# Kernel optimization log

Measured on AMD Instinct MI355X. Metric: run time of the kernel, lower is better.

Reference implementation:

```python
import jax, jax.numpy as jnp
import numpy as np

NUM_HEADS = 4
NUM_GROUPS = 8
EPS = 1e-5


def group_norm(x, w, b):
    # x: [B, C, H, W], 8 groups, per-channel affine
    B, C, H, W = x.shape
    g = x.reshape(B, NUM_GROUPS, C // NUM_GROUPS, H, W)
    mu = g.mean(axis=(2, 3, 4), keepdims=True)
    var = g.var(axis=(2, 3, 4), keepdims=True)
    g = (g - mu) * jax.lax.rsqrt(var + EPS)
    x = g.reshape(B, C, H, W)
    return x * w[None, :, None, None] + b[None, :, None, None]


def setup_inputs() -> dict:
    key = jax.random.key(0)
    ks = jax.random.split(key, 7)
    B, C, H, W = 16, 256, 32, 32
    x = jax.random.normal(ks[0], (B, C, H, W), dtype=jnp.float32)
    norm_w = jnp.ones((C,), jnp.float32)
    norm_b = jnp.zeros((C,), jnp.float32)
    # 1x1 convs == channel matmuls; fan-in scaled init
    qkv_w = jax.random.normal(ks[1], (3 * C, C), dtype=jnp.float32) / np.sqrt(C)
    qkv_b = jnp.zeros((3 * C,), jnp.float32)
    proj_w = jax.random.normal(ks[2], (C, C), dtype=jnp.float32) / np.sqrt(C)
    proj_b = jnp.zeros((C,), jnp.float32)
    return {"x": x, "norm_w": norm_w, "norm_b": norm_b,
            "qkv_w": qkv_w, "qkv_b": qkv_b,
            "proj_w": proj_w, "proj_b": proj_b}


def reference(x, norm_w, norm_b, qkv_w, qkv_b, proj_w, proj_b):
    B, C, H, W = x.shape
    nh = NUM_HEADS
    d = C // nh
    N = H * W

    h = group_norm(x, norm_w, norm_b)
    # 1x1 conv -> channel matmul: [B, 3C, H, W]
    qkv = jnp.einsum('oc,bchw->bohw', qkv_w, h) + qkv_b[None, :, None, None]
    qkv = qkv.reshape(B, 3, nh, d, N)
    q, k, v = qkv[:, 0], qkv[:, 1], qkv[:, 2]  # [B, nh, d, N]

    scale = d ** (-0.5)
    attn = jnp.einsum('bhcn,bhcm->bhnm', q, k) * scale  # [B, nh, N, N]
    attn = jax.nn.softmax(attn, axis=-1)
    out = jnp.einsum('bhnm,bhcm->bhcn', attn, v)  # [B, nh, d, N]
    out = out.reshape(B, C, H, W)
    out = jnp.einsum('oc,bchw->bohw', proj_w, out) + proj_b[None, :, None, None]
    return x + out
```

## Files before the change

kernel.cpp:

```cpp
#include <hip/hip_runtime.h>
#include <math.h>

#define BATCH 16
#define CH 256
#define NG 8
#define NH 4
#define HD 64
#define NN 1024
#define GSZ 32
#define GELEMS (GSZ * NN)

typedef __attribute__((ext_vector_type(8))) __bf16 bf16x8;
typedef __attribute__((ext_vector_type(4))) __bf16 bf16x4;
typedef __attribute__((ext_vector_type(4))) _Float16 f16x4;
typedef __attribute__((ext_vector_type(4))) float f32x4;

__device__ __forceinline__ unsigned short f2b(float f) {
    union { __bf16 h; unsigned short u; } c; c.h = (__bf16)f; return c.u;
}
__device__ __forceinline__ unsigned short f2h(float f) {
    union { _Float16 h; unsigned short u; } c; c.h = (_Float16)f; return c.u;
}

#define MFMA(a, b, c) __builtin_amdgcn_mfma_f32_16x16x32_bf16(a, b, c, 0, 0, 0)
#define MFMA16(a, b, c) __builtin_amdgcn_mfma_f32_16x16x16f16(a, b, c, 0, 0, 0)

__global__ __launch_bounds__(256) void gnw_kernel(
    const float* __restrict__ x, const float* __restrict__ w,
    const float* __restrict__ bb, const float* __restrict__ qkv_w,
    const float* __restrict__ proj_w, unsigned short* __restrict__ hT,
    unsigned short* __restrict__ wq, unsigned short* __restrict__ wp)
{
    int tid = threadIdx.x;
    if (blockIdx.x >= 128) {
        int t = (blockIdx.x - 128) * 256 + tid;
        const float* src; unsigned short* dst; size_t off;
        if (t < 24576) { src = qkv_w; dst = wq; off = (size_t)t * 8; }
        else           { src = proj_w; dst = wp; off = (size_t)(t - 24576) * 8; }
        const float4* s4 = (const float4*)(src + off);
        float4 a = s4[0], b = s4[1];
        bf16x8 pk;
        pk[0] = (__bf16)a.x; pk[1] = (__bf16)a.y; pk[2] = (__bf16)a.z; pk[3] = (__bf16)a.w;
        pk[4] = (__bf16)b.x; pk[5] = (__bf16)b.y; pk[6] = (__bf16)b.z; pk[7] = (__bf16)b.w;
        *(bf16x8*)(dst + off) = pk;
        return;
    }
    const int b = blockIdx.x >> 3, g = blockIdx.x & 7;
    const float* xb = x + ((size_t)b * CH + g * GSZ) * NN;
    const float4* x4 = (const float4*)xb;

    float s = 0.f, ss = 0.f;
    #pragma unroll
    for (int i = 0; i < 32; ++i) {
        float4 v = x4[tid + i * 256];
        s  += v.x + v.y + v.z + v.w;
        ss += v.x * v.x + v.y * v.y + v.z * v.z + v.w * v.w;
    }
    #pragma unroll
    for (int off = 1; off < 64; off <<= 1) {
        s  += __shfl_xor(s, off);
        ss += __shfl_xor(ss, off);
    }
    __shared__ float red[8];
    int wave = tid >> 6, lane = tid & 63;
    if (lane == 0) { red[wave] = s; red[4 + wave] = ss; }
    __syncthreads();
    if (tid == 0) {
        float ts  = red[0] + red[1] + red[2] + red[3];
        float tss = red[4] + red[5] + red[6] + red[7];
        float mu  = ts * (1.f / GELEMS);
        float var = tss * (1.f / GELEMS) - mu * mu;
        red[0] = mu; red[1] = rsqrtf(var + 1e-5f);
    }
    __syncthreads();
    const float mu = red[0], rs = red[1];

    const int co = tid & 3;
    float wcv[8], bcv[8];
    #pragma unroll
    for (int j = 0; j < 8; ++j) {
        int c = g * GSZ + co * 8 + j;
        wcv[j] = w[c] * rs;
        bcv[j] = bb[c] - mu * wcv[j];
    }
    __shared__ float Ts[32][66];
    const int cs = tid >> 3, q = tid & 7;
    const int n_l = tid >> 2;
    for (int nt = 0; nt < 16; ++nt) {
        const float2* src = (const float2*)(xb + (size_t)cs * NN + nt * 64 + q * 8);
        #pragma unroll
        for (int t = 0; t < 4; ++t)
            *(float2*)&Ts[cs][q * 8 + t * 2] = src[t];
        __syncthreads();
        bf16x8 pk;
        #pragma unroll
        for (int j = 0; j < 8; ++j)
            pk[j] = (__bf16)(Ts[co * 8 + j][n_l] * wcv[j] + bcv[j]);
        *(bf16x8*)(hT + ((size_t)b * NN + nt * 64 + n_l) * CH + g * GSZ + co * 8) = pk;
        __syncthreads();
    }
}

template <int KIND>
__global__ __launch_bounds__(256) void gemm_kernel(
    const unsigned short* __restrict__ AT,
    const unsigned short* __restrict__ Wb,
    const float* __restrict__ bias,
    unsigned short* __restrict__ outT, unsigned short* __restrict__ outV,
    const float* __restrict__ res, float* __restrict__ out)
{
    __shared__ __align__(16) unsigned short Ws[64][136];
    __shared__ __align__(16) unsigned short Hs[64][136];
    const int b = blockIdx.z, o0 = blockIdx.y * 64, n0 = blockIdx.x * 64;
    const int tid = threadIdx.x;
    const int lane = tid & 63, wv = tid >> 6;
    const int l = lane & 15, quad = lane >> 4;
    const int iw = wv & 1, jw = wv >> 1;
    const bool qk_mode = (KIND == 0) && (blockIdx.y < 8);
    const bool v_mode  = (KIND == 0) && (blockIdx.y >= 8);
    const int r4 = tid >> 2, c4 = tid & 3;

    f32x4 acc[2][2] = {};
    for (int st = 0; st < 2; ++st) {
        const int cc0 = st * 128;
        #pragma unroll
        for (int i = 0; i < 4; ++i) {
            int ch = c4 + i * 4;
            *(bf16x8*)&Ws[r4][ch * 8] =
                *(const bf16x8*)(Wb + (size_t)(o0 + r4) * CH + cc0 + ch * 8);
            *(bf16x8*)&Hs[r4][ch * 8] =
                *(const bf16x8*)(AT + ((size_t)b * NN + n0 + r4) * CH + cc0 + ch * 8);
        }
        __syncthreads();
        #pragma unroll
        for (int kt = 0; kt < 4; ++kt) {
            bf16x8 af[2], bf[2];
            #pragma unroll
            for (int i = 0; i < 2; ++i)
                af[i] = *(const bf16x8*)&Hs[iw * 32 + i * 16 + l][kt * 32 + quad * 8];
            #pragma unroll
            for (int j = 0; j < 2; ++j)
                bf[j] = *(const bf16x8*)&Ws[jw * 32 + j * 16 + l][kt * 32 + quad * 8];
            #pragma unroll
            for (int i = 0; i < 2; ++i)
                #pragma unroll
                for (int j = 0; j < 2; ++j)
                    acc[i][j] = v_mode ? MFMA(af[i], bf[j], acc[i][j])
                                       : MFMA(bf[j], af[i], acc[i][j]);
        }
        __syncthreads();
    }

    unsigned short* Cs = (unsigned short*)Ws;
    if (qk_mode) {
        #pragma unroll
        for (int i = 0; i < 2; ++i)
            #pragma unroll
            for (int j = 0; j < 2; ++j) {
                int o_p = jw * 32 + j * 16 + quad * 4;
                int n_l = iw * 32 + i * 16 + l;
                bf16x4 pk;
                #pragma unroll
                for (int r = 0; r < 4; ++r)
                    pk[r] = (__bf16)(acc[i][j][r] + bias[o0 + o_p + r]);
                *(bf16x4*)&Cs[n_l * 72 + o_p] = pk;
            }
        __syncthreads();
        int rr = tid >> 2, ch = tid & 3;
        bf16x8 a0 = *(const bf16x8*)&Cs[rr * 72 + ch * 16];
        bf16x8 a1 = *(const bf16x8*)&Cs[rr * 72 + ch * 16 + 8];
        unsigned short* dst = outT + ((size_t)b * NN + n0 + rr) * 512 + o0 + ch * 16;
        *(bf16x8*)dst = a0;
        *(bf16x8*)(dst + 8) = a1;
    } else if (v_mode) {
        #pragma unroll
        for (int i = 0; i < 2; ++i)
            #pragma unroll
            for (int j = 0; j < 2; ++j) {
                int n_p = iw * 32 + i * 16 + quad * 4;
                int o_l = jw * 32 + j * 16 + l;
                float bs = bias[o0 + o_l];
                f16x4 pk;
                #pragma unroll
                for (int r = 0; r < 4; ++r)
                    pk[r] = (_Float16)(acc[i][j][r] + bs);
                *(f16x4*)&Cs[o_l * 72 + n_p] = pk;
            }
        __syncthreads();
        int rr = tid >> 2, ch = tid & 3;
        bf16x8 a0 = *(const bf16x8*)&Cs[rr * 72 + ch * 16];
        bf16x8 a1 = *(const bf16x8*)&Cs[rr * 72 + ch * 16 + 8];
        unsigned short* dst = outV + ((size_t)b * CH + (o0 + rr - 512)) * NN + n0 + ch * 16;
        *(bf16x8*)dst = a0;
        *(bf16x8*)(dst + 8) = a1;
    } else {
        #pragma unroll
        for (int i = 0; i < 2; ++i)
            #pragma unroll
            for (int j = 0; j < 2; ++j) {
                int o = o0 + jw * 32 + j * 16 + quad * 4;
                int n = n0 + iw * 32 + i * 16 + l;
                #pragma unroll
                for (int r = 0; r < 4; ++r) {
                    size_t idx = ((size_t)b * CH + o + r) * NN + n;
                    out[idx] = acc[i][j][r] + bias[o + r] + res[idx];
                }
            }
    }
}

__global__ __launch_bounds__(256, 4) void attn_kernel(
    const unsigned short* __restrict__ qkvT,
    const unsigned short* __restrict__ vbuf,
    unsigned short* __restrict__ ctxT)
{
    __shared__ __align__(16) unsigned short KV[2][8192];
    __shared__ float Lred[2][32];
    const int id = blockIdx.x;
    const int bh = id & 63, nt = id >> 6;
    const int b = bh >> 2, hh = bh & 3;
    const int n0 = nt * 64;
    const int tid = threadIdx.x;
    const int lane = tid & 63, w = tid >> 6;
    const int l = lane & 15, quad = lane >> 4;
    const int qx = w & 1, ky = w >> 1;
    const float KL2E = 0.125f * 1.44269504f;
    const int r4 = tid >> 2, c4 = tid & 3;

    bf16x8 qf[2][2];
    {
        const unsigned short* qp = qkvT + ((size_t)b * NN + n0 + 32 * qx + l) * 512 + hh * 64;
        #pragma unroll
        for (int ns = 0; ns < 2; ++ns)
            #pragma unroll
            for (int kt = 0; kt < 2; ++kt)
                qf[ns][kt] = *(const bf16x8*)(qp + (size_t)ns * 16 * 512 + kt * 32 + quad * 8);
    }

    const unsigned short* gk = qkvT + ((size_t)b * NN + r4) * 512 + 256 + hh * 64;
    const unsigned short* gv = vbuf + ((size_t)b * CH + hh * 64 + r4) * NN;
    const int p0 = (c4 ^ (r4 & 7)) * 8, p1 = ((c4 + 4) ^ (r4 & 7)) * 8;

    bf16x8 kpre0, kpre1, vpre0, vpre1;
    kpre0 = *(const bf16x8*)(gk + c4 * 8);
    kpre1 = *(const bf16x8*)(gk + (c4 + 4) * 8);
    vpre0 = *(const bf16x8*)(gv + c4 * 8);
    vpre1 = *(const bf16x8*)(gv + (c4 + 4) * 8);
    *(bf16x8*)&KV[0][r4 * 64 + p0] = kpre0;
    *(bf16x8*)&KV[0][r4 * 64 + p1] = kpre1;
    *(bf16x8*)&KV[0][4096 + r4 * 64 + p0] = vpre0;
    *(bf16x8*)&KV[0][4096 + r4 * 64 + p1] = vpre1;
    __syncthreads();

    float l_w[2] = {0.f, 0.f};
    f32x4 oacc[2][4] = {};

    for (int mt = 0; mt < 16; ++mt) {
        const int cur = mt & 1;
        if (mt < 15) {
            const unsigned short* gk1 = gk + (size_t)(mt + 1) * 64 * 512;
            const unsigned short* gv1 = gv + (mt + 1) * 64;
            kpre0 = *(const bf16x8*)(gk1 + c4 * 8);
            kpre1 = *(const bf16x8*)(gk1 + (c4 + 4) * 8);
            vpre0 = *(const bf16x8*)(gv1 + c4 * 8);
            vpre1 = *(const bf16x8*)(gv1 + (c4 + 4) * 8);
        }

        bf16x8 kf[2][2];
        #pragma unroll
        for (int mt2 = 0; mt2 < 2; ++mt2)
            #pragma unroll
            for (int kt = 0; kt < 2; ++kt)
                kf[mt2][kt] = *(const bf16x8*)
                    &KV[cur][(32 * ky + 16 * mt2 + l) * 64 + (((kt * 4 + quad) ^ (l & 7)) * 8)];

        f32x4 sacc[2][2] = {};
        #pragma unroll
        for (int kt = 0; kt < 2; ++kt)
            #pragma unroll
            for (int mt2 = 0; mt2 < 2; ++mt2)
                #pragma unroll
                for (int ns = 0; ns < 2; ++ns)
                    sacc[mt2][ns] = MFMA(kf[mt2][kt], qf[ns][kt], sacc[mt2][ns]);

        f16x4 pf[2][2];
        #pragma unroll
        for (int mt2 = 0; mt2 < 2; ++mt2)
            #pragma unroll
            for (int ns = 0; ns < 2; ++ns)
                #pragma unroll
                for (int r = 0; r < 4; ++r) {
                    float p = exp2f(sacc[mt2][ns][r] * KL2E);
                    l_w[ns] += p;
                    pf[mt2][ns][r] = (_Float16)p;
                }

        #pragma unroll
        for (int mt2 = 0; mt2 < 2; ++mt2) {
            const int q8 = 4 * ky + 2 * mt2 + (quad >> 1);
            const int vo = ((q8 ^ (l & 7)) * 8) + (quad & 1) * 4;
            #pragma unroll
            for (int ct = 0; ct < 4; ++ct) {
                f16x4 va = *(const f16x4*)&KV[cur][4096 + (16 * ct + l) * 64 + vo];
                #pragma unroll
                for (int ns = 0; ns < 2; ++ns)
                    oacc[ns][ct] = MFMA16(va, pf[mt2][ns], oacc[ns][ct]);
            }
        }

        if (mt < 15) {
            const int nxt = cur ^ 1;
            *(bf16x8*)&KV[nxt][r4 * 64 + p0] = kpre0;
            *(bf16x8*)&KV[nxt][r4 * 64 + p1] = kpre1;
            *(bf16x8*)&KV[nxt][4096 + r4 * 64 + p0] = vpre0;
            *(bf16x8*)&KV[nxt][4096 + r4 * 64 + p1] = vpre1;
            __syncthreads();
        }
    }

    #pragma unroll
    for (int ns = 0; ns < 2; ++ns) {
        l_w[ns] += __shfl_xor(l_w[ns], 16);
        l_w[ns] += __shfl_xor(l_w[ns], 32);
    }
    float* Ored = (float*)&KV[0][0];
    if (ky == 1) {
        #pragma unroll
        for (int ns = 0; ns < 2; ++ns) {
            if (quad == 0) Lred[qx][ns * 16 + l] = l_w[ns];
            #pragma unroll
            for (int ct = 0; ct < 4; ++ct)
                #pragma unroll
                for (int r = 0; r < 4; ++r)
                    Ored[qx * 2048 + (16 * ct + quad * 4 + r) * 32 + ns * 16 + l] =
                        oacc[ns][ct][r];
        }
    }
    __syncthreads();
    if (ky == 0) {
        unsigned short* cb = ctxT + ((size_t)b * NN + n0 + 32 * qx) * CH + hh * 64;
        #pragma unroll
        for (int ns = 0; ns < 2; ++ns) {
            float inv = 1.f / (l_w[ns] + Lred[qx][ns * 16 + l]);
            #pragma unroll
            for (int ct = 0; ct < 4; ++ct) {
                bf16x4 pk;
                #pragma unroll
                for (int r = 0; r < 4; ++r)
                    pk[r] = (__bf16)((oacc[ns][ct][r] +
                             Ored[qx * 2048 + (16 * ct + quad * 4 + r) * 32 + ns * 16 + l]) * inv);
                *(bf16x4*)(cb + (size_t)(ns * 16 + l) * CH + 16 * ct + quad * 4) = pk;
            }
        }
    }
}

extern "C" void kernel_launch(void* const* d_in, const int* in_sizes, int n_in,
                              void* d_out, int out_size, void* d_ws, size_t ws_size,
                              hipStream_t stream)
{
    const float* x      = (const float*)d_in[0];
    const float* norm_w = (const float*)d_in[1];
    const float* norm_b = (const float*)d_in[2];
    const float* qkv_w  = (const float*)d_in[3];
    const float* qkv_b  = (const float*)d_in[4];
    const float* proj_w = (const float*)d_in[5];
    const float* proj_b = (const float*)d_in[6];
    float* out = (float*)d_out;

    unsigned short* hT   = (unsigned short*)d_ws;
    unsigned short* qkvT = hT   + (size_t)BATCH * NN * CH;
    unsigned short* vbuf = qkvT + (size_t)BATCH * NN * 512;
    unsigned short* ctxT = vbuf + (size_t)BATCH * CH * NN;
    unsigned short* wq   = ctxT + (size_t)BATCH * NN * CH;
    unsigned short* wp   = wq + (size_t)768 * CH;

    gnw_kernel<<<dim3(256), 256, 0, stream>>>(x, norm_w, norm_b, qkv_w, proj_w, hT, wq, wp);
    gemm_kernel<0><<<dim3(NN / 64, 12, BATCH), 256, 0, stream>>>(
        hT, wq, qkv_b, qkvT, vbuf, nullptr, nullptr);
    attn_kernel<<<dim3(1024), 256, 0, stream>>>(qkvT, vbuf, ctxT);
    gemm_kernel<1><<<dim3(NN / 64, 4, BATCH), 256, 0, stream>>>(
        ctxT, wp, proj_b, nullptr, nullptr, x, out);
}
```

Before: 145.8 us.

## Split QKV GEMM into dedicated kernel with 128-row tiles and XOR-swizzled LDS

Replaces the templated GEMM with a dedicated QKV kernel that uses 128x64 output tiles over four 64-wide K chunks, staging operands in XOR-swizzled shared memory instead of padded rows. This halves the grid along N, doubles weight reuse per block and is meant to cut LDS bank conflicts. The group-norm transpose now stages with float4 loads into a 68-wide pad. The cost is more accumulators per thread and fewer blocks in flight.

```diff
diff --git a/kernel.cpp b/kernel.cpp
--- a/kernel.cpp
+++ b/kernel.cpp
@@ -83,14 +83,13 @@
         wcv[j] = w[c] * rs;
         bcv[j] = bb[c] - mu * wcv[j];
     }
-    __shared__ float Ts[32][66];
+    __shared__ float Ts[32][68];
     const int cs = tid >> 3, q = tid & 7;
     const int n_l = tid >> 2;
     for (int nt = 0; nt < 16; ++nt) {
-        const float2* src = (const float2*)(xb + (size_t)cs * NN + nt * 64 + q * 8);
-        #pragma unroll
-        for (int t = 0; t < 4; ++t)
-            *(float2*)&Ts[cs][q * 8 + t * 2] = src[t];
+        const float4* src = (const float4*)(xb + (size_t)cs * NN + nt * 64 + q * 8);
+        *(float4*)&Ts[cs][q * 8]     = src[0];
+        *(float4*)&Ts[cs][q * 8 + 4] = src[1];
         __syncthreads();
         bf16x8 pk;
         #pragma unroll
@@ -101,12 +100,111 @@
     }
 }
 
-template <int KIND>
-__global__ __launch_bounds__(256) void gemm_kernel(
+__global__ __launch_bounds__(256) void gemm_qkv(
     const unsigned short* __restrict__ AT,
     const unsigned short* __restrict__ Wb,
     const float* __restrict__ bias,
-    unsigned short* __restrict__ outT, unsigned short* __restrict__ outV,
+    unsigned short* __restrict__ outT, unsigned short* __restrict__ outV)
+{
+    __shared__ __align__(16) unsigned short S[128 * 64 + 64 * 64];
+    unsigned short* As = S;
+    unsigned short* Wl = S + 128 * 64;
+    const int b = blockIdx.z, o0 = blockIdx.y * 64, n0 = blockIdx.x * 128;
+    const int tid = threadIdx.x;
+    const int lane = tid & 63, w = tid >> 6;
+    const int l = lane & 15, quad = lane >> 4;
+    const int iw = w & 1, jw = w >> 1;
+    const bool qk_mode = (blockIdx.y < 8);
+    const int sr = tid >> 2, sc = tid & 3;
+
+    f32x4 acc[4][2] = {};
+    for (int cc = 0; cc < 4; ++cc) {
+        const int cc0 = cc * 64;
+        #pragma unroll
+        for (int i = 0; i < 2; ++i) {
+            int r = sr + i * 64;
+            const unsigned short* ga = AT + ((size_t)b * NN + n0 + r) * CH + cc0;
+            *(bf16x8*)&As[r * 64 + ((sc ^ (r & 7)) * 8)] = *(const bf16x8*)(ga + sc * 8);
+            *(bf16x8*)&As[r * 64 + (((sc + 4) ^ (r & 7)) * 8)] = *(const bf16x8*)(ga + (sc + 4) * 8);
+        }
+        {
+            const unsigned short* gw = Wb + (size_t)(o0 + sr) * CH + cc0;
+            *(bf16x8*)&Wl[sr * 64 + ((sc ^ (sr & 7)) * 8)] = *(const bf16x8*)(gw + sc * 8);
+            *(bf16x8*)&Wl[sr * 64 + (((sc + 4) ^ (sr & 7)) * 8)] = *(const bf16x8*)(gw + (sc + 4) * 8);
+        }
+        __syncthreads();
+        #pragma unroll
+        for (int kt = 0; kt < 2; ++kt) {
+            const int q = ((kt * 4 + quad) ^ (l & 7)) * 8;
+            bf16x8 af[4], bf[2];
+            #pragma unroll
+            for (int i = 0; i < 4; ++i)
+                af[i] = *(const bf16x8*)&As[(iw * 64 + i * 16 + l) * 64 + q];
+            #pragma unroll
+            for (int j = 0; j < 2; ++j)
+                bf[j] = *(const bf16x8*)&Wl[(jw * 32 + j * 16 + l) * 64 + q];
+            #pragma unroll
+            for (int i = 0; i < 4; ++i)
+                #pragma unroll
+                for (int j = 0; j < 2; ++j)
+                    acc[i][j] = qk_mode ? MFMA(bf[j], af[i], acc[i][j])
+                                        : MFMA(af[i], bf[j], acc[i][j]);
+        }
+        __syncthreads();
+    }
+
+    if (qk_mode) {
+        unsigned short* Cs = S;
+        #pragma unroll
+        for (int i = 0; i < 4; ++i)
+            #pragma unroll
+            for (int j = 0; j < 2; ++j) {
+                int o_p = jw * 32 + j * 16 + quad * 4;
+                int n_l = iw * 64 + i * 16 + l;
+                bf16x4 pk;
+                #pragma unroll
+                for (int r = 0; r < 4; ++r)
+                    pk[r] = (__bf16)(acc[i][j][r] + bias[o0 + o_p + r]);
+                *(bf16x4*)&Cs[n_l * 72 + o_p] = pk;
+            }
+        __syncthreads();
+        int rr = tid >> 1, hf = tid & 1;
+        unsigned short* dst = outT + ((size_t)b * NN + n0 + rr) * 512 + o0 + hf * 32;
+        const unsigned short* srcp = &Cs[rr * 72 + hf * 32];
+        *(bf16x8*)dst = *(const bf16x8*)srcp;
+        *(bf16x8*)(dst + 8) = *(const bf16x8*)(srcp + 8);
+        *(bf16x8*)(dst + 16) = *(const bf16x8*)(srcp + 16);
+        *(bf16x8*)(dst + 24) = *(const bf16x8*)(srcp + 24);
+    } else {
+        unsigned short* Cs = S;
+        #pragma unroll
+        for (int i = 0; i < 4; ++i)
+            #pragma unroll
+            for (int j = 0; j < 2; ++j) {
+                int n_p = iw * 64 + i * 16 + quad * 4;
+                int o_l = jw * 32 + j * 16 + l;
+                float bs = bias[o0 + o_l];
+                f16x4 pk;
+                #pragma unroll
+                for (int r = 0; r < 4; ++r)
+                    pk[r] = (_Float16)(acc[i][j][r] + bs);
+                *(f16x4*)&Cs[o_l * 136 + n_p] = pk;
+            }
+        __syncthreads();
+        int rr = tid >> 2, ch = tid & 3;
+        unsigned short* dst = outV + ((size_t)b * CH + (o0 + rr - 512)) * NN + n0 + ch * 32;
+        const unsigned short* srcp = &Cs[rr * 136 + ch * 32];
+        *(bf16x8*)dst = *(const bf16x8*)srcp;
+        *(bf16x8*)(dst + 8) = *(const bf16x8*)(srcp + 8);
+        *(bf16x8*)(dst + 16) = *(const bf16x8*)(srcp + 16);
+        *(bf16x8*)(dst + 24) = *(const bf16x8*)(srcp + 24);
+    }
+}
+
+__global__ __launch_bounds__(256) void gemm_proj(
+    const unsigned short* __restrict__ AT,
+    const unsigned short* __restrict__ Wb,
+    const float* __restrict__ bias,
     const float* __restrict__ res, float* __restrict__ out)
 {
     __shared__ __align__(16) unsigned short Ws[64][136];
@@ -116,8 +214,6 @@
     const int lane = tid & 63, wv = tid >> 6;
     const int l = lane & 15, quad = lane >> 4;
     const int iw = wv & 1, jw = wv >> 1;
-    const bool qk_mode = (KIND == 0) && (blockIdx.y < 8);
-    const bool v_mode  = (KIND == 0) && (blockIdx.y >= 8);
     const int r4 = tid >> 2, c4 = tid & 3;
 
     f32x4 acc[2][2] = {};
@@ -145,68 +241,22 @@
             for (int i = 0; i < 2; ++i)
                 #pragma unroll
                 for (int j = 0; j < 2; ++j)
-                    acc[i][j] = v_mode ? MFMA(af[i], bf[j], acc[i][j])
-                                       : MFMA(bf[j], af[i], acc[i][j]);
-        }
-        __syncthreads();
-    }
-
-    unsigned short* Cs = (unsigned short*)Ws;
-    if (qk_mode) {
-        #pragma unroll
-        for (int i = 0; i < 2; ++i)
-            #pragma unroll
-            for (int j = 0; j < 2; ++j) {
-                int o_p = jw * 32 + j * 16 + quad * 4;
-                int n_l = iw * 32 + i * 16 + l;
-                bf16x4 pk;
-                #pragma unroll
-                for (int r = 0; r < 4; ++r)
-                    pk[r] = (__bf16)(acc[i][j][r] + bias[o0 + o_p + r]);
-                *(bf16x4*)&Cs[n_l * 72 + o_p] = pk;
+                    acc[i][j] = MFMA(bf[j], af[i], acc[i][j]);
+        }
+        __syncthreads();
+    }
+    #pragma unroll
+    for (int i = 0; i < 2; ++i)
+        #pragma unroll
+        for (int j = 0; j < 2; ++j) {
+            int o = o0 + jw * 32 + j * 16 + quad * 4;
+            int n = n0 + iw * 32 + i * 16 + l;
+            #pragma unroll
+            for (int r = 0; r < 4; ++r) {
+                size_t idx = ((size_t)b * CH + o + r) * NN + n;
+                out[idx] = acc[i][j][r] + bias[o + r] + res[idx];
             }
-        __syncthreads();
-        int rr = tid >> 2, ch = tid & 3;
-        bf16x8 a0 = *(const bf16x8*)&Cs[rr * 72 + ch * 16];
-        bf16x8 a1 = *(const bf16x8*)&Cs[rr * 72 + ch * 16 + 8];
-        unsigned short* dst = outT + ((size_t)b * NN + n0 + rr) * 512 + o0 + ch * 16;
-        *(bf16x8*)dst = a0;
-        *(bf16x8*)(dst + 8) = a1;
-    } else if (v_mode) {
-        #pragma unroll
-        for (int i = 0; i < 2; ++i)
-            #pragma unroll
-            for (int j = 0; j < 2; ++j) {
-                int n_p = iw * 32 + i * 16 + quad * 4;
-                int o_l = jw * 32 + j * 16 + l;
-                float bs = bias[o0 + o_l];
-                f16x4 pk;
-                #pragma unroll
-                for (int r = 0; r < 4; ++r)
-                    pk[r] = (_Float16)(acc[i][j][r] + bs);
-                *(f16x4*)&Cs[o_l * 72 + n_p] = pk;
-            }
-        __syncthreads();
-        int rr = tid >> 2, ch = tid & 3;
-        bf16x8 a0 = *(const bf16x8*)&Cs[rr * 72 + ch * 16];
-        bf16x8 a1 = *(const bf16x8*)&Cs[rr * 72 + ch * 16 + 8];
-        unsigned short* dst = outV + ((size_t)b * CH + (o0 + rr - 512)) * NN + n0 + ch * 16;
-        *(bf16x8*)dst = a0;
-        *(bf16x8*)(dst + 8) = a1;
-    } else {
-        #pragma unroll
-        for (int i = 0; i < 2; ++i)
-            #pragma unroll
-            for (int j = 0; j < 2; ++j) {
-                int o = o0 + jw * 32 + j * 16 + quad * 4;
-                int n = n0 + iw * 32 + i * 16 + l;
-                #pragma unroll
-                for (int r = 0; r < 4; ++r) {
-                    size_t idx = ((size_t)b * CH + o + r) * NN + n;
-                    out[idx] = acc[i][j][r] + bias[o + r] + res[idx];
-                }
-            }
-    }
+        }
 }
 
 __global__ __launch_bounds__(256, 4) void attn_kernel(
@@ -376,9 +426,7 @@
     unsigned short* wp   = wq + (size_t)768 * CH;
 
     gnw_kernel<<<dim3(256), 256, 0, stream>>>(x, norm_w, norm_b, qkv_w, proj_w, hT, wq, wp);
-    gemm_kernel<0><<<dim3(NN / 64, 12, BATCH), 256, 0, stream>>>(
-        hT, wq, qkv_b, qkvT, vbuf, nullptr, nullptr);
+    gemm_qkv<<<dim3(8, 12, BATCH), 256, 0, stream>>>(hT, wq, qkv_b, qkvT, vbuf);
     attn_kernel<<<dim3(1024), 256, 0, stream>>>(qkvT, vbuf, ctxT);
-    gemm_kernel<1><<<dim3(NN / 64, 4, BATCH), 256, 0, stream>>>(
-        ctxT, wp, proj_b, nullptr, nullptr, x, out);
-}
+    gemm_proj<<<dim3(16, 4, BATCH), 256, 0, stream>>>(ctxT, wp, proj_b, x, out);
+}
```

New measurement: 149.7 us. 2.6% more time.
